# Kernel optimization log

Hardware: AMD Instinct MI355X
Metric: run time of the kernel (lower is better)

## Reference

```python
import jax, jax.numpy as jnp
import numpy as np

EPS_NORM = 1e-12  # F.normalize eps
EPS_BN = 1e-5     # BatchNorm2d eps


def _neighbor_idx(h, w):
    # Replicates get_window_mask's clamped 3x3 neighbor indices (hw, 9).
    off = np.array([-1, 0, 1])
    x_off = np.tile(off, 3)        # [-1,0,1,-1,0,1,-1,0,1]
    y_off = np.repeat(off, 3)      # [-1,-1,-1,0,0,0,1,1,1]
    yy, xx = np.meshgrid(np.arange(h), np.arange(w), indexing='ij')
    x_nn = np.clip(xx.reshape(-1, 1) + x_off[None, :], 0, w - 1)
    y_nn = np.clip(yy.reshape(-1, 1) + y_off[None, :], 0, h - 1)
    return jnp.asarray(y_nn * w + x_nn, dtype=jnp.int32)  # (hw, 9)


def _find_nn(xf, yf, idx):
    # Faithful to find_nn: cosine sim between cur pixel and 3x3 window of y,
    # argmin over the (masked-in) window, gather the NORMALIZED y feature.
    # The dense (hw,hw) matmul + 9999 mask reduces exactly to these 9 candidates.
    b, c, h, w = xf.shape
    xn = xf.reshape(b, c, h * w).transpose(0, 2, 1)  # (b, hw, c)
    xn = xn / jnp.maximum(jnp.linalg.norm(xn, axis=-1, keepdims=True), EPS_NORM)
    yn = yf.reshape(b, c, h * w)
    yn = yn / jnp.maximum(jnp.linalg.norm(yn, axis=1, keepdims=True), EPS_NORM)
    ynt = yn.transpose(0, 2, 1)          # (b, hw, c)
    y_nb = ynt[:, idx, :]                # (b, hw, 9, c) gathered neighbors
    sims = jnp.einsum('bpc,bpkc->bpk', xn, y_nb)  # (b, hw, 9)
    k = jnp.argmin(sims, axis=-1)
    nnv = jnp.take_along_axis(y_nb, k[:, :, None, None], axis=2)[:, :, 0, :]
    return nnv.transpose(0, 2, 1).reshape(b, c, h, w)


def _forward(x, conv_w, bn_gamma, bn_beta):
    h, w = x.shape[-2:]
    prev_f, next_f, cur_f = x[:, 0], x[:, 1], x[:, 2]
    idx = _neighbor_idx(h, w)
    nn_prev = _find_nn(cur_f, prev_f, idx)
    nn_next = _find_nn(cur_f, next_f, idx)
    feat = jnp.concatenate([nn_prev, nn_next, cur_f], axis=1)  # (b, 3c, h, w)
    out = jnp.einsum('oc,bchw->bohw', conv_w, feat)            # 1x1 conv, no bias
    # BatchNorm2d in training mode: per-channel batch stats (biased var)
    mean = out.mean(axis=(0, 2, 3), keepdims=True)
    var = out.var(axis=(0, 2, 3), keepdims=True)
    out = (out - mean) * jax.lax.rsqrt(var + EPS_BN)
    out = out * bn_gamma[None, :, None, None] + bn_beta[None, :, None, None]
    out = jax.nn.relu(out)
    return jnp.stack([prev_f, next_f, out], axis=1)  # (b, 3, c, h, w)


def setup_inputs() -> dict:
    key = jax.random.key(0)
    k1, k2 = jax.random.split(key)
    b, c, h, w = 8, 256, 64, 64
    x = jax.random.normal(k1, (b, 3, c, h, w), dtype=jnp.float32)
    fan_in, fan_out = 3 * c, c
    bound = float(np.sqrt(6.0 / (fan_in + fan_out)))  # xavier_uniform
    conv_w = jax.random.uniform(k2, (c, 3 * c), dtype=jnp.float32, minval=-bound, maxval=bound)
    bn_gamma = jnp.ones((c,), dtype=jnp.float32)
    bn_beta = jnp.zeros((c,), dtype=jnp.float32)
    return {'x': x, 'conv_w': conv_w, 'bn_gamma': bn_gamma, 'bn_beta': bn_beta}


def reference(x, conv_w, bn_gamma, bn_beta):
    return _forward(x, conv_w, bn_gamma, bn_beta)
```

## Files before the change

### kernel.cpp

```cpp
#include <hip/hip_runtime.h>

constexpr int B  = 8;
constexpr int C  = 256;
constexpr int Hh = 64;
constexpr int Ww = 64;
constexpr int P  = Hh * Ww;
constexpr int CP = C * P;
constexpr int CT = 3 * C;
constexpr int J  = B * P;

constexpr int DOT_D_OFF = 0;
constexpr int SSQ_D_OFF = 294912;
constexpr int SEL_F_OFF = 663552;
constexpr int SIV_F_OFF = 671744;
constexpr int WB_F_OFF  = 679936;
constexpr int BNS_D_OFF = 389120;

typedef __attribute__((ext_vector_type(8))) short short8;
typedef __attribute__((ext_vector_type(4))) float f32x4;

__device__ inline unsigned short bf16_rne(float f) {
    unsigned u = __float_as_uint(f);
    return (unsigned short)((u + 0x7fffu + ((u >> 16) & 1u)) >> 16);
}
__device__ inline unsigned pack2(float a, float b) {
    return (unsigned)bf16_rne(a) | ((unsigned)bf16_rne(b) << 16);
}

__global__ __launch_bounds__(256) void k_wcvt(const float* __restrict__ Wg,
                                              unsigned short* __restrict__ Wb,
                                              float* __restrict__ out) {
    int i = blockIdx.x * 256 + threadIdx.x;
    Wb[i] = bf16_rne(Wg[i]);
    if (blockIdx.x == 0) {
        double* bns = (double*)out + BNS_D_OFF;
        bns[threadIdx.x]       = 0.0;
        bns[256 + threadIdx.x] = 0.0;
    }
}

__global__ __launch_bounds__(256) void k_dots(const float* __restrict__ x,
                                              float* __restrict__ out) {
    __shared__ float ys[2][2][2][6][64];
    __shared__ float cs[2][2][256];
    const int t     = threadIdx.x;
    const int b     = blockIdx.x >> 4;
    const int strip = blockIdx.x & 15;
    const int chunk = blockIdx.y;
    const int y0 = strip * 4;
    const int ry = t >> 6;
    const int xc = t & 63;
    const int xm = max(xc - 1, 0), xp = min(xc + 1, 63);
    const int c0 = chunk * 64;

    size_t gbase;
    float *d00, *d01, *d10, *d11;
    float* ysf = &ys[0][0][0][0][0];
    float* csf = &cs[0][0][0];
    if (t < 64) {
        gbase = (size_t)(b * 3 + 2) * CP + (size_t)c0 * P + strip * 256 + t * 4;
        int l0 = t * 4;
        d00 = csf + l0;        d01 = csf + 256 + l0;
        d10 = csf + 512 + l0;  d11 = csf + 768 + l0;
    } else {
        int i   = t - 64;
        int sid = i >= 96;
        int r   = (i - sid * 96) >> 4;
        int x4  = i & 15;
        int yl  = min(max(y0 - 1 + r, 0), Hh - 1);
        gbase = (size_t)(b * 3 + sid) * CP + (size_t)c0 * P + yl * 64 + x4 * 4;
        int l0 = (sid * 6 + r) * 64 + x4 * 4;
        d00 = ysf + l0;         d01 = ysf + 768 + l0;
        d10 = ysf + 1536 + l0;  d11 = ysf + 1536 + 768 + l0;
    }

    double d[2][9] = {{0,0,0,0,0,0,0,0,0},{0,0,0,0,0,0,0,0,0}};
    double qs[2] = {0.0, 0.0};

    f32x4 a0 = *(const f32x4*)(x + gbase);
    f32x4 a1 = *(const f32x4*)(x + gbase + (size_t)P);
    f32x4 b0 = *(const f32x4*)(x + gbase + (size_t)2 * P);
    f32x4 b1 = *(const f32x4*)(x + gbase + (size_t)3 * P);

    #define COMPUTE(BUF, CH)                                                 \
    {                                                                        \
        double cd = (double)cs[BUF][CH][t];                                  \
        _Pragma("unroll")                                                    \
        for (int s = 0; s < 2; ++s) {                                        \
            const float* Y0 = &ys[BUF][CH][s][ry][0];         \
            const float* Y1 = Y0 + 64;                        \
            const float* Y2 = Y1 + 64;                        \
            d[s][0] = fma(cd, (double)Y0[xm], d[s][0]);                      \
            d[s][1] = fma(cd, (double)Y0[xc], d[s][1]);                      \
            d[s][2] = fma(cd, (double)Y0[xp], d[s][2]);                      \
            d[s][3] = fma(cd, (double)Y1[xm], d[s][3]);                      \
            d[s][4] = fma(cd, (double)Y1[xc], d[s][4]);                      \
            d[s][5] = fma(cd, (double)Y1[xp], d[s][5]);                      \
            d[s][6] = fma(cd, (double)Y2[xm], d[s][6]);                      \
            d[s][7] = fma(cd, (double)Y2[xc], d[s][7]);                      \
            d[s][8] = fma(cd, (double)Y2[xp], d[s][8]);                      \
            double ov = (double)Y1[xc];                                      \
            qs[s] = fma(ov, ov, qs[s]);                                      \
        }                                                                    \
    }

    for (int n = 0; n < 64; n += 4) {
        *(f32x4*)d00 = a0; *(f32x4*)d01 = a1;
        __syncthreads();
        if (n + 4 < 64) {
            a0 = *(const f32x4*)(x + gbase + (size_t)(n + 4) * P);
            a1 = *(const f32x4*)(x + gbase + (size_t)(n + 5) * P);
        }
        COMPUTE(0, 0) COMPUTE(0, 1)
        *(f32x4*)d10 = b0; *(f32x4*)d11 = b1;
        __syncthreads();
        if (n + 6 < 64) {
            b0 = *(const f32x4*)(x + gbase + (size_t)(n + 6) * P);
            b1 = *(const f32x4*)(x + gbase + (size_t)(n + 7) * P);
        }
        COMPUTE(1, 0) COMPUTE(1, 1)
    }
    #undef COMPUTE

    const int p = strip * 256 + t;
    double* db = (double*)(out + (size_t)(b * 3) * CP);
    #pragma unroll
    for (int s = 0; s < 2; ++s) {
        #pragma unroll
        for (int k = 0; k < 9; ++k)
            db[DOT_D_OFF + (size_t)((chunk * 2 + s) * 9 + k) * 4096 + p] = d[s][k];
        db[SSQ_D_OFF + (size_t)(chunk * 2 + s) * 4096 + p] = qs[s];
    }
}

__global__ __launch_bounds__(256) void k_sel(float* __restrict__ out) {
    int gid  = blockIdx.x * 256 + threadIdx.x;
    int side = gid >> 15;
    int j    = gid & (J - 1);
    int b = j >> 12, p = j & (P - 1);
    int y = p >> 6, xc = p & 63;

    int nidx[9];
    #pragma unroll
    for (int k = 0; k < 9; ++k) {
        int dy = k / 3 - 1, dx = k % 3 - 1;
        int yy = min(max(y + dy, 0), Hh - 1);
        int xx = min(max(xc + dx, 0), Ww - 1);
        nidx[k] = yy * Ww + xx;
    }

    const double* db = (const double*)(out + (size_t)(b * 3) * CP) + DOT_D_OFF;
    const double* sb = (const double*)(out + (size_t)(b * 3) * CP) + SSQ_D_OFF;

    double best = 0.0; int bi = 0; float sivbest = 0.0f;
    #pragma unroll
    for (int k = 0; k < 9; ++k) {
        int nq = nidx[k];
        double ssum = ((sb[(0 * 2 + side) * 4096 + nq]
                      + sb[(1 * 2 + side) * 4096 + nq])
                      + sb[(2 * 2 + side) * 4096 + nq])
                      + sb[(3 * 2 + side) * 4096 + nq];
        float ivf = 1.0f / fmaxf((float)sqrt(ssum), 1e-12f);
        double sk = ((db[(size_t)((0 * 2 + side) * 9 + k) * 4096 + p]
                    + db[(size_t)((1 * 2 + side) * 9 + k) * 4096 + p])
                    + db[(size_t)((2 * 2 + side) * 9 + k) * 4096 + p])
                    + db[(size_t)((3 * 2 + side) * 9 + k) * 4096 + p];
        double s = sk * (double)ivf;
        if (k == 0 || s < best) { best = s; bi = k; sivbest = ivf; }
    }
    int*   selb = (int*)(out + (size_t)(b * 3) * CP + SEL_F_OFF);
    float* sivb = out + (size_t)(b * 3) * CP + SIV_F_OFF;
    selb[side * 4096 + p] = nidx[bi];
    sivb[side * 4096 + p] = sivbest;
}

__global__ __launch_bounds__(512) void k_gemm(const float* __restrict__ x,
                                              const unsigned short* __restrict__ Wb,
                                              float* __restrict__ out) {
    __shared__ unsigned short As[2][4][256][8];
    __shared__ unsigned short Bs[2][4][128][8];
    __shared__ int   sel_s[2][128];
    __shared__ float siv_s[2][128];
    __shared__ float sw_s[8][64], sw_q[8][64];

    const int t  = threadIdx.x;
    const int j0 = blockIdx.x * 128;
    const int b  = j0 >> 12, p0 = j0 & (P - 1);

    if (t < 256) {
        int side = t >> 7, jj = t & 127;
        const int*   selb = (const int*)(out + (size_t)(b * 3) * CP + SEL_F_OFF);
        const float* sivb = out + (size_t)(b * 3) * CP + SIV_F_OFF;
        sel_s[side][jj] = selb[side * 4096 + p0 + jj];
        siv_s[side][jj] = sivb[side * 4096 + p0 + jj];
    }
    __syncthreads();

    const int lane = t & 63, w = t >> 6;
    const int q = lane >> 4, l16 = lane & 15;
    const int m0w = (w & 3) * 64;
    const int n0w = (w >> 2) * 64;

    const int jj = t & 127, kq = (t >> 7) & 3;
    const int ma = t & 255, kh = t >> 8;
    const int k0 = kq * 8;

    const float* pp = x + (size_t)(b * 3 + 0) * CP + sel_s[0][jj];
    const float* np = x + (size_t)(b * 3 + 1) * CP + sel_s[1][jj];
    const float* cp = x + (size_t)(b * 3 + 2) * CP + p0 + jj;
    const float  sp = siv_s[0][jj], sn = siv_s[1][jj];
    const unsigned short* wbase = Wb + (size_t)ma * CT + kh * 16;

    f32x4 acc[4][4];
    #pragma unroll
    for (int f = 0; f < 4; ++f)
        #pragma unroll
        for (int g = 0; g < 4; ++g)
            acc[f][g] = (f32x4){0.f, 0.f, 0.f, 0.f};

    short8 wa0, wa1;
    float fb[8];
    float scale;

    #define LOAD_STEP(KK)                                                    \
    {                                                                        \
        const unsigned short* wsrc = wbase + (KK);                           \
        wa0 = *(const short8*)wsrc;                                          \
        wa1 = *(const short8*)(wsrc + 8);                                    \
        const float* src;                                                    \
        if ((KK) < 256)      { src = pp + (size_t)((KK) + k0) * P;       scale = sp;   } \
        else if ((KK) < 512) { src = np + (size_t)((KK) - 256 + k0) * P; scale = sn;   } \
        else                 { src = cp + (size_t)((KK) - 512 + k0) * P; scale = 1.0f; } \
        _Pragma("unroll")                                                    \
        for (int u = 0; u < 8; ++u) fb[u] = src[(size_t)u * P];              \
    }

    #define WRITE_STEP(BUF)                                                  \
    {                                                                        \
        *(short8*)&As[BUF][kh * 2    ][ma][0] = wa0;                         \
        *(short8*)&As[BUF][kh * 2 + 1][ma][0] = wa1;                         \
        uint4 pk = make_uint4(pack2(fb[0] * scale, fb[1] * scale),           \
                              pack2(fb[2] * scale, fb[3] * scale),           \
                              pack2(fb[4] * scale, fb[5] * scale),           \
                              pack2(fb[6] * scale, fb[7] * scale));          \
        *(uint4*)&Bs[BUF][kq][jj][0] = pk;                                   \
    }

    LOAD_STEP(0)
    WRITE_STEP(0)
    __syncthreads();

    for (int i = 0; i < 24; ++i) {
        if (i + 1 < 24) LOAD_STEP((i + 1) * 32)
        const int cur = i & 1;
        short8 af[4], bfr[4];
        #pragma unroll
        for (int f = 0; f < 4; ++f)
            af[f] = *(const short8*)&As[cur][q][m0w + f * 16 + l16][0];
        #pragma unroll
        for (int g = 0; g < 4; ++g)
            bfr[g] = *(const short8*)&Bs[cur][q][n0w + g * 16 + l16][0];
        #pragma unroll
        for (int f = 0; f < 4; ++f)
            #pragma unroll
            for (int g = 0; g < 4; ++g)
                acc[f][g] = __builtin_amdgcn_mfma_f32_16x16x32_bf16(
                    af[f], bfr[g], acc[f][g], 0, 0, 0);
        if (i + 1 < 24) WRITE_STEP((i + 1) & 1)
        __syncthreads();
    }
    #undef LOAD_STEP
    #undef WRITE_STEP

    float* outb = out + (size_t)(b * 3 + 2) * CP;
    #pragma unroll
    for (int f = 0; f < 4; ++f)
        #pragma unroll
        for (int g = 0; g < 4; ++g)
            #pragma unroll
            for (int r = 0; r < 4; ++r) {
                int ch  = m0w + f * 16 + q * 4 + r;
                int col = p0 + n0w + g * 16 + l16;
                outb[(size_t)ch * P + col] = acc[f][g][r];
            }

    #pragma unroll
    for (int f = 0; f < 4; ++f)
        #pragma unroll
        for (int r = 0; r < 4; ++r) {
            float s  = acc[f][0][r] + acc[f][1][r] + acc[f][2][r] + acc[f][3][r];
            float qq = acc[f][0][r] * acc[f][0][r] + acc[f][1][r] * acc[f][1][r]
                     + acc[f][2][r] * acc[f][2][r] + acc[f][3][r] * acc[f][3][r];
            #pragma unroll
            for (int m = 1; m <= 8; m <<= 1) {
                s  += __shfl_xor(s, m);
                qq += __shfl_xor(qq, m);
            }
            if (l16 == 0) {
                sw_s[w][f * 16 + q * 4 + r] = s;
                sw_q[w][f * 16 + q * 4 + r] = qq;
            }
        }
    __syncthreads();
    if (t < 256) {
        int quad = t >> 6, lch = t & 63;
        double s  = (double)sw_s[quad][lch] + (double)sw_s[4 + quad][lch];
        double qq = (double)sw_q[quad][lch] + (double)sw_q[4 + quad][lch];
        double* bns = (double*)out + BNS_D_OFF;
        atomicAdd(&bns[t], s);
        atomicAdd(&bns[256 + t], qq);
    }
}

__global__ __launch_bounds__(256) void k_bn(float* __restrict__ out,
                                            const float* __restrict__ gamma,
                                            const float* __restrict__ beta) {
    const int o = blockIdx.x, t = threadIdx.x;
    const double* bns = (const double*)out + BNS_D_OFF;
    double mean = bns[o] * (1.0 / (double)J);
    double var  = bns[256 + o] * (1.0 / (double)J) - mean * mean;
    double inv  = 1.0 / sqrt(var + 1e-5);
    double scd  = (double)gamma[o] * inv;
    const float sc = (float)scd;
    const float sh = (float)((double)beta[o] - mean * scd);

    for (int b = 0; b < B; ++b) {
        float4* base =
            (float4*)(out + (size_t)(b * 3 + 2) * CP + (size_t)o * P);
        #pragma unroll
        for (int i = 0; i < 4; ++i) {
            float4 v = base[i * 256 + t];
            v.x = fmaxf(fmaf(v.x, sc, sh), 0.f);
            v.y = fmaxf(fmaf(v.y, sc, sh), 0.f);
            v.z = fmaxf(fmaf(v.z, sc, sh), 0.f);
            v.w = fmaxf(fmaf(v.w, sc, sh), 0.f);
            base[i * 256 + t] = v;
        }
    }
}

__global__ __launch_bounds__(256) void k_copy(const float4* __restrict__ x4,
                                              float4* __restrict__ o4) {
    int tid = blockIdx.x * blockDim.x + threadIdx.x;
    const int per_b = 2 * CP / 4;
    const int bstr  = 3 * CP / 4;
    if (tid < B * per_b) {
        int b = tid / per_b;
        int r = tid - b * per_b;
        o4[b * bstr + r] = x4[b * bstr + r];
    }
}

extern "C" void kernel_launch(void* const* d_in, const int* in_sizes, int n_in,
                              void* d_out, int out_size, void* d_ws, size_t ws_size,
                              hipStream_t stream) {
    const float* x     = (const float*)d_in[0];
    const float* wconv = (const float*)d_in[1];
    const float* gamma = (const float*)d_in[2];
    const float* beta  = (const float*)d_in[3];
    float* out = (float*)d_out;
    (void)d_ws; (void)ws_size;

    unsigned short* Wbuf = (unsigned short*)(out + WB_F_OFF);

    k_wcvt<<<CT * C / 256, 256, 0, stream>>>(wconv, Wbuf, out);

    k_dots<<<dim3(128, 4), 256, 0, stream>>>(x, out);

    k_sel<<<2 * J / 256, 256, 0, stream>>>(out);

    k_gemm<<<J / 128, 512, 0, stream>>>(x, Wbuf, out);

    k_bn<<<C, 256, 0, stream>>>(out, gamma, beta);

    k_copy<<<(B * 2 * CP / 4 + 255) / 256, 256, 0, stream>>>(
        (const float4*)x, (float4*)out);
}
```

Measured before the change: 257.3 us.

## Fold weight conversion into dots kernel and selection into GEMM prologue

The bf16 weight conversion and BN-stat zeroing move into k_dots: each of its 512 blocks converts 384 weight elements. The argmin neighbor selection moves into the GEMM kernel's prologue, which reads the partial dot and sum-of-squares buffers directly into shared memory. This removes two kernel launches and the global round trip for the sel/siv arrays. In exchange, the GEMM prologue does more serial work with scattered double loads before its first barrier.

```diff
diff --git a/kernel.cpp b/kernel.cpp
--- a/kernel.cpp
+++ b/kernel.cpp
@@ -11,8 +11,6 @@
 
 constexpr int DOT_D_OFF = 0;
 constexpr int SSQ_D_OFF = 294912;
-constexpr int SEL_F_OFF = 663552;
-constexpr int SIV_F_OFF = 671744;
 constexpr int WB_F_OFF  = 679936;
 constexpr int BNS_D_OFF = 389120;
 
@@ -27,19 +25,8 @@
     return (unsigned)bf16_rne(a) | ((unsigned)bf16_rne(b) << 16);
 }
 
-__global__ __launch_bounds__(256) void k_wcvt(const float* __restrict__ Wg,
-                                              unsigned short* __restrict__ Wb,
-                                              float* __restrict__ out) {
-    int i = blockIdx.x * 256 + threadIdx.x;
-    Wb[i] = bf16_rne(Wg[i]);
-    if (blockIdx.x == 0) {
-        double* bns = (double*)out + BNS_D_OFF;
-        bns[threadIdx.x]       = 0.0;
-        bns[256 + threadIdx.x] = 0.0;
-    }
-}
-
 __global__ __launch_bounds__(256) void k_dots(const float* __restrict__ x,
+                                              const float* __restrict__ Wg,
                                               float* __restrict__ out) {
     __shared__ float ys[2][2][2][6][64];
     __shared__ float cs[2][2][256];
@@ -47,6 +34,19 @@
     const int b     = blockIdx.x >> 4;
     const int strip = blockIdx.x & 15;
     const int chunk = blockIdx.y;
+
+    {
+        int lid  = blockIdx.y * 128 + blockIdx.x;
+        int base = lid * 384;
+        unsigned short* Wb = (unsigned short*)(out + WB_F_OFF);
+        Wb[base + t] = bf16_rne(Wg[base + t]);
+        if (t < 128) Wb[base + 256 + t] = bf16_rne(Wg[base + 256 + t]);
+        if (lid == 0) {
+            double* bns = (double*)out + BNS_D_OFF;
+            bns[t] = 0.0; bns[256 + t] = 0.0;
+        }
+    }
+
     const int y0 = strip * 4;
     const int ry = t >> 6;
     const int xc = t & 63;
@@ -133,49 +133,7 @@
     }
 }
 
-__global__ __launch_bounds__(256) void k_sel(float* __restrict__ out) {
-    int gid  = blockIdx.x * 256 + threadIdx.x;
-    int side = gid >> 15;
-    int j    = gid & (J - 1);
-    int b = j >> 12, p = j & (P - 1);
-    int y = p >> 6, xc = p & 63;
-
-    int nidx[9];
-    #pragma unroll
-    for (int k = 0; k < 9; ++k) {
-        int dy = k / 3 - 1, dx = k % 3 - 1;
-        int yy = min(max(y + dy, 0), Hh - 1);
-        int xx = min(max(xc + dx, 0), Ww - 1);
-        nidx[k] = yy * Ww + xx;
-    }
-
-    const double* db = (const double*)(out + (size_t)(b * 3) * CP) + DOT_D_OFF;
-    const double* sb = (const double*)(out + (size_t)(b * 3) * CP) + SSQ_D_OFF;
-
-    double best = 0.0; int bi = 0; float sivbest = 0.0f;
-    #pragma unroll
-    for (int k = 0; k < 9; ++k) {
-        int nq = nidx[k];
-        double ssum = ((sb[(0 * 2 + side) * 4096 + nq]
-                      + sb[(1 * 2 + side) * 4096 + nq])
-                      + sb[(2 * 2 + side) * 4096 + nq])
-                      + sb[(3 * 2 + side) * 4096 + nq];
-        float ivf = 1.0f / fmaxf((float)sqrt(ssum), 1e-12f);
-        double sk = ((db[(size_t)((0 * 2 + side) * 9 + k) * 4096 + p]
-                    + db[(size_t)((1 * 2 + side) * 9 + k) * 4096 + p])
-                    + db[(size_t)((2 * 2 + side) * 9 + k) * 4096 + p])
-                    + db[(size_t)((3 * 2 + side) * 9 + k) * 4096 + p];
-        double s = sk * (double)ivf;
-        if (k == 0 || s < best) { best = s; bi = k; sivbest = ivf; }
-    }
-    int*   selb = (int*)(out + (size_t)(b * 3) * CP + SEL_F_OFF);
-    float* sivb = out + (size_t)(b * 3) * CP + SIV_F_OFF;
-    selb[side * 4096 + p] = nidx[bi];
-    sivb[side * 4096 + p] = sivbest;
-}
-
 __global__ __launch_bounds__(512) void k_gemm(const float* __restrict__ x,
-                                              const unsigned short* __restrict__ Wb,
                                               float* __restrict__ out) {
     __shared__ unsigned short As[2][4][256][8];
     __shared__ unsigned short Bs[2][4][128][8];
@@ -186,13 +144,40 @@
     const int t  = threadIdx.x;
     const int j0 = blockIdx.x * 128;
     const int b  = j0 >> 12, p0 = j0 & (P - 1);
+    const unsigned short* Wb = (const unsigned short*)(out + WB_F_OFF);
 
     if (t < 256) {
         int side = t >> 7, jj = t & 127;
-        const int*   selb = (const int*)(out + (size_t)(b * 3) * CP + SEL_F_OFF);
-        const float* sivb = out + (size_t)(b * 3) * CP + SIV_F_OFF;
-        sel_s[side][jj] = selb[side * 4096 + p0 + jj];
-        siv_s[side][jj] = sivb[side * 4096 + p0 + jj];
+        int p = p0 + jj;
+        int y = p >> 6, xc = p & 63;
+        int nidx[9];
+        #pragma unroll
+        for (int k = 0; k < 9; ++k) {
+            int dy = k / 3 - 1, dx = k % 3 - 1;
+            int yy = min(max(y + dy, 0), Hh - 1);
+            int xx = min(max(xc + dx, 0), Ww - 1);
+            nidx[k] = yy * Ww + xx;
+        }
+        const double* db = (const double*)(out + (size_t)(b * 3) * CP) + DOT_D_OFF;
+        const double* sb = (const double*)(out + (size_t)(b * 3) * CP) + SSQ_D_OFF;
+        double best = 0.0; int bi = 0; float sivbest = 0.0f;
+        #pragma unroll
+        for (int k = 0; k < 9; ++k) {
+            int nq = nidx[k];
+            double ssum = ((sb[(0 * 2 + side) * 4096 + nq]
+                          + sb[(1 * 2 + side) * 4096 + nq])
+                          + sb[(2 * 2 + side) * 4096 + nq])
+                          + sb[(3 * 2 + side) * 4096 + nq];
+            float ivf = 1.0f / fmaxf((float)sqrt(ssum), 1e-12f);
+            double sk = ((db[(size_t)((0 * 2 + side) * 9 + k) * 4096 + p]
+                        + db[(size_t)((1 * 2 + side) * 9 + k) * 4096 + p])
+                        + db[(size_t)((2 * 2 + side) * 9 + k) * 4096 + p])
+                        + db[(size_t)((3 * 2 + side) * 9 + k) * 4096 + p];
+            double s = sk * (double)ivf;
+            if (k == 0 || s < best) { best = s; bi = k; sivbest = ivf; }
+        }
+        sel_s[side][jj] = nidx[bi];
+        siv_s[side][jj] = sivbest;
     }
     __syncthreads();
 
@@ -361,15 +346,9 @@
     float* out = (float*)d_out;
     (void)d_ws; (void)ws_size;
 
-    unsigned short* Wbuf = (unsigned short*)(out + WB_F_OFF);
-
-    k_wcvt<<<CT * C / 256, 256, 0, stream>>>(wconv, Wbuf, out);
-
-    k_dots<<<dim3(128, 4), 256, 0, stream>>>(x, out);
-
-    k_sel<<<2 * J / 256, 256, 0, stream>>>(out);
-
-    k_gemm<<<J / 128, 512, 0, stream>>>(x, Wbuf, out);
+    k_dots<<<dim3(128, 4), 256, 0, stream>>>(x, wconv, out);
+
+    k_gemm<<<J / 128, 512, 0, stream>>>(x, out);
 
     k_bn<<<C, 256, 0, stream>>>(out, gamma, beta);
 
```

Measured after the change: 253.6 us. Within noise of the previous version (-1.5%).
